# Kernel tuning notes

Measured on AMD Instinct MI355X. Metric: run time of the kernel, lower is better.

## Reference

```python
import jax, jax.numpy as jnp
import numpy as np

EPS = 1e-12


def setup_inputs() -> dict:
    key = jax.random.key(0)
    k1, k2, k3, k4 = jax.random.split(key, 4)
    N, H, W, D, K = 64, 32, 32, 512, 64
    x = jax.random.normal(k1, (N, H, W, D), dtype=jnp.float32)
    W_assign = jax.random.normal(k2, (D, K), dtype=jnp.float32) * 0.05  # 1x1 conv kernel
    b_assign = jax.random.normal(k3, (K,), dtype=jnp.float32) * 0.05
    C = jax.random.normal(k4, (D, K), dtype=jnp.float32) * 0.05  # cluster centers
    return {"x": x, "W_assign": W_assign, "b_assign": b_assign, "C": C}


def _l2norm(v, axis):
    return v / jnp.sqrt(jnp.sum(v * v, axis=axis, keepdims=True) + EPS)


def reference(x, W_assign, b_assign, C):
    # 1x1 conv = matmul over channel dim: [N,H,W,D] @ [D,K] -> [N,H,W,K]
    s = jnp.einsum('nhwd,dk->nhwk', x, W_assign) + b_assign
    a = jax.nn.softmax(s, axis=-1)                       # soft assignment over K
    # VLAD: v[n,d,k] = sum_hw a[n,h,w,k] * (x[n,h,w,d] + C[d,k])
    # reformulated as two small contractions (no [N,H,W,D,K] intermediate):
    v = jnp.einsum('nhwd,nhwk->ndk', x, a)               # feature-weighted sums
    a_sum = jnp.sum(a, axis=(1, 2))                      # [N,K]
    v = v + a_sum[:, None, :] * C[None, :, :]            # [N,D,K]
    # intra-normalization: L2 over D per cluster (after transpose to [N,K,D])
    v = _l2norm(jnp.transpose(v, (0, 2, 1)), axis=-1)    # [N,K,D]
    v = jnp.transpose(v, (0, 2, 1))                      # [N,D,K]
    # flatten and final L2 normalize -> [N, D*K]
    v = v.reshape(v.shape[0], -1)
    return _l2norm(v, axis=-1)
```

## Files before the change

kernel.cpp:

```cpp
#include <hip/hip_runtime.h>


#define EPSF 1e-12f

typedef short bf16x8 __attribute__((ext_vector_type(8)));
typedef float f32x16 __attribute__((ext_vector_type(16)));

__device__ inline unsigned short f2bf_rne(float f) {
  union { float f; unsigned u; } v; v.f = f;
  unsigned u = v.u;
  unsigned r = u + 0x7fffu + ((u >> 16) & 1u);
  return (unsigned short)(r >> 16);
}
__device__ inline unsigned pk2(float a, float b) {
  return (unsigned)f2bf_rne(a) | ((unsigned)f2bf_rne(b) << 16);
}

__global__ __launch_bounds__(256) void kprep(
    const float* __restrict__ Wm, unsigned short* __restrict__ wt) {
  __shared__ float tile[64][65];
  const int t = threadIdx.x, bx = blockIdx.x;
  {
    int col = (t & 15) * 4, rbase = t >> 4;
#pragma unroll
    for (int r = 0; r < 4; ++r) {
      int row = rbase + 16 * r;
      *(float4*)&tile[row][col] =
          *(const float4*)&Wm[(size_t)(bx * 64 + row) * 64 + col];
    }
  }
  __syncthreads();
  int k = t >> 2, seg = (t & 3) * 16;
  size_t o = (size_t)k * 512 + bx * 64 + seg;
#pragma unroll
  for (int j = 0; j < 16; j += 2)
    *(unsigned*)&wt[o + j] = pk2(tile[seg + j][k], tile[seg + j + 1][k]);
}

__global__ __launch_bounds__(256) void kassign(
    const float* __restrict__ x, const unsigned short* __restrict__ wt,
    const float* __restrict__ b, unsigned short* __restrict__ at,
    float* __restrict__ a_sum) {
  __shared__ unsigned short xs[128][72];
  __shared__ unsigned short ws[64][72];
  const int t = threadIdx.x;
  const int w = t >> 6, lane = t & 63, l31 = lane & 31, h = lane >> 5;
  const int p0 = blockIdx.x * 128;
  const int col = (t & 15) * 4, rbase = t >> 4;
  const int wk = t >> 2, wseg = (t & 3) * 16;

  float4 px[8];
  uint4 pw0, pw1;
#pragma unroll
  for (int r = 0; r < 8; ++r)
    px[r] = *(const float4*)&x[(size_t)(p0 + rbase + 16 * r) * 512 + col];
  pw0 = *(const uint4*)&wt[(size_t)wk * 512 + wseg];
  pw1 = *(const uint4*)&wt[(size_t)wk * 512 + wseg + 8];

  f32x16 acc0, acc1;
#pragma unroll
  for (int i = 0; i < 16; ++i) { acc0[i] = 0.f; acc1[i] = 0.f; }

  for (int c = 0; c < 8; ++c) {
    __syncthreads();
#pragma unroll
    for (int r = 0; r < 8; ++r) {
      uint2 ph;
      ph.x = pk2(px[r].x, px[r].y);
      ph.y = pk2(px[r].z, px[r].w);
      *(uint2*)&xs[rbase + 16 * r][col] = ph;
    }
    *(uint4*)&ws[wk][wseg] = pw0;
    *(uint4*)&ws[wk][wseg + 8] = pw1;
    __syncthreads();
    if (c < 7) {
      const int dc = (c + 1) * 64;
#pragma unroll
      for (int r = 0; r < 8; ++r)
        px[r] = *(const float4*)&x[(size_t)(p0 + rbase + 16 * r) * 512 + dc + col];
      pw0 = *(const uint4*)&wt[(size_t)wk * 512 + dc + wseg];
      pw1 = *(const uint4*)&wt[(size_t)wk * 512 + dc + wseg + 8];
    }
#pragma unroll
    for (int s = 0; s < 4; ++s) {
      int kd = s * 16 + h * 8;
      bf16x8 ax = *(const bf16x8*)&xs[32 * w + l31][kd];
      bf16x8 b0 = *(const bf16x8*)&ws[l31][kd];
      bf16x8 b1 = *(const bf16x8*)&ws[32 + l31][kd];
      acc0 = __builtin_amdgcn_mfma_f32_32x32x16_bf16(ax, b0, acc0, 0, 0, 0);
      acc1 = __builtin_amdgcn_mfma_f32_32x32x16_bf16(ax, b1, acc1, 0, 0, 0);
    }
  }

  const float bias0 = b[l31], bias1 = b[32 + l31];
  float a0[16], a1[16];
  float sum0 = 0.f, sum1 = 0.f;
#pragma unroll
  for (int r = 0; r < 16; ++r) {
    float s0 = acc0[r] + bias0, s1 = acc1[r] + bias1;
    float m = fmaxf(s0, s1);
#pragma unroll
    for (int msk = 1; msk < 32; msk <<= 1) m = fmaxf(m, __shfl_xor(m, msk, 64));
    float e0 = __expf(s0 - m), e1 = __expf(s1 - m);
    float S = e0 + e1;
#pragma unroll
    for (int msk = 1; msk < 32; msk <<= 1) S += __shfl_xor(S, msk, 64);
    float inv = 1.0f / S;
    a0[r] = e0 * inv; a1[r] = e1 * inv;
    sum0 += a0[r]; sum1 += a1[r];
  }
  const int n = p0 >> 10;
  const int hwb = (p0 & 1023) + 32 * w + 4 * h;
  const size_t kb0 = ((size_t)n * 64 + l31) * 1024;
  const size_t kb1 = ((size_t)n * 64 + 32 + l31) * 1024;
#pragma unroll
  for (int g = 0; g < 4; ++g) {
    int hw = hwb + 8 * g;
    uint2 u;
    u.x = pk2(a0[4 * g + 0], a0[4 * g + 1]);
    u.y = pk2(a0[4 * g + 2], a0[4 * g + 3]);
    *(uint2*)&at[kb0 + hw] = u;
    u.x = pk2(a1[4 * g + 0], a1[4 * g + 1]);
    u.y = pk2(a1[4 * g + 2], a1[4 * g + 3]);
    *(uint2*)&at[kb1 + hw] = u;
  }
  sum0 += __shfl_xor(sum0, 32, 64);
  sum1 += __shfl_xor(sum1, 32, 64);
  if (lane < 32) {
    atomicAdd(&a_sum[n * 64 + l31], sum0);
    atomicAdd(&a_sum[n * 64 + 32 + l31], sum1);
  }
}

__global__ __launch_bounds__(256) void kvlad(
    const float* __restrict__ x, const unsigned short* __restrict__ at,
    const float* __restrict__ a_sum, const float* __restrict__ C,
    float* __restrict__ out, float* __restrict__ ssq) {
  __shared__ float xs[64][68];
  __shared__ unsigned short as_[64][72];
  const int t = threadIdx.x;
  const int w = t >> 6, lane = t & 63, l31 = lane & 31, h = lane >> 5;
  const int n = blockIdx.y, d0 = blockIdx.x * 64;
  const int dw = 32 * (w & 1), kw = 32 * (w >> 1);
  const float* xb = x + (size_t)n * 1024 * 512;
  const int col = (t & 15) * 4, rbase = t >> 4;
  const int ak = t >> 2, aseg = (t & 3) * 16;
  const size_t abase = ((size_t)n * 64 + ak) * 1024;

  float4 px[4];
  uint4 pa0, pa1;
#pragma unroll
  for (int r = 0; r < 4; ++r)
    px[r] = *(const float4*)&xb[(size_t)(rbase + 16 * r) * 512 + d0 + col];
  pa0 = *(const uint4*)&at[abase + aseg];
  pa1 = *(const uint4*)&at[abase + aseg + 8];

  f32x16 acc;
#pragma unroll
  for (int i = 0; i < 16; ++i) acc[i] = 0.f;

  for (int c = 0; c < 16; ++c) {
    __syncthreads();
#pragma unroll
    for (int r = 0; r < 4; ++r)
      *(float4*)&xs[rbase + 16 * r][col] = px[r];
    *(uint4*)&as_[ak][aseg] = pa0;
    *(uint4*)&as_[ak][aseg + 8] = pa1;
    __syncthreads();
    if (c < 15) {
      const int hw0 = (c + 1) * 64;
#pragma unroll
      for (int r = 0; r < 4; ++r)
        px[r] = *(const float4*)&xb[(size_t)(hw0 + rbase + 16 * r) * 512 + d0 + col];
      pa0 = *(const uint4*)&at[abase + hw0 + aseg];
      pa1 = *(const uint4*)&at[abase + hw0 + aseg + 8];
    }
#pragma unroll
    for (int s = 0; s < 4; ++s) {
      int kk = s * 16 + h * 8;
      bf16x8 ax;
#pragma unroll
      for (int j = 0; j < 8; ++j)
        ax[j] = (short)f2bf_rne(xs[kk + j][dw + l31]);
      bf16x8 bh = *(const bf16x8*)&as_[kw + l31][kk];
      acc = __builtin_amdgcn_mfma_f32_32x32x16_bf16(ax, bh, acc, 0, 0, 0);
    }
  }

  const int k = kw + l31;
  const float as = a_sum[n * 64 + k];
  float sq = 0.f;
#pragma unroll
  for (int r = 0; r < 16; ++r) {
    int row = (r & 3) + 8 * (r >> 2) + 4 * h;
    int d = d0 + dw + row;
    float o = acc[r] + as * C[(size_t)d * 64 + k];
    out[((size_t)n * 512 + d) * 64 + k] = o;
    sq += o * o;
  }
  atomicAdd(&ssq[n * 64 + k], sq);
}

__global__ __launch_bounds__(256) void kscale(
    float* __restrict__ out, const float* __restrict__ ssq) {
  const int n = blockIdx.y, slice = blockIdx.x;
  const int t = threadIdx.x, k = t & 63, rg = t >> 6;
  __shared__ float sk[64];
  __shared__ float tot;
  if (t < 64) {
    float c = ssq[n * 64 + t];
    sk[t] = rsqrtf(c + EPSF);
    float contrib = c / (c + EPSF);
#pragma unroll
    for (int m = 32; m; m >>= 1) contrib += __shfl_xor(contrib, m, 64);
    if (t == 0) tot = rsqrtf(contrib + EPSF);
  }
  __syncthreads();
  const float scale = sk[k] * tot;
  float* vb = out + (size_t)n * 32768 + (size_t)slice * 4096;
#pragma unroll
  for (int r = rg; r < 64; r += 4) vb[r * 64 + k] *= scale;
}

extern "C" void kernel_launch(void* const* d_in, const int* in_sizes, int n_in,
                              void* d_out, int out_size, void* d_ws, size_t ws_size,
                              hipStream_t stream) {
  const float* x  = (const float*)d_in[0];
  const float* Wm = (const float*)d_in[1];
  const float* b  = (const float*)d_in[2];
  const float* C  = (const float*)d_in[3];
  float* out = (float*)d_out;

  unsigned short* at = (unsigned short*)d_ws;
  unsigned short* wt = at + (size_t)64 * 64 * 1024;
  float* a_sum = (float*)(wt + (size_t)64 * 512);
  float* ssq   = a_sum + 4096;

  hipMemsetAsync(a_sum, 0, 8192 * sizeof(float), stream);
  kprep<<<dim3(8), dim3(256), 0, stream>>>(Wm, wt);
  kassign<<<dim3(512), dim3(256), 0, stream>>>(x, wt, b, at, a_sum);
  kvlad<<<dim3(8, 64), dim3(256), 0, stream>>>(x, at, a_sum, C, out, ssq);
  kscale<<<dim3(8, 64), dim3(256), 0, stream>>>(out, ssq);
}
```

Baseline: 274.4 us.

## Pre-transpose x to bf16 [N,D,HW] layout for the VLAD contraction

Adds a kernel that converts x to bf16 and transposes it to a D-major, HW-contiguous layout in workspace. The VLAD kernel then loads bf16 rows with vector LDS reads, replacing strided fp32 LDS reads and per-element bf16 conversion in the inner loop. This costs an extra full pass over x (128 MB read, 64 MB written) while kvlad reads half as many bytes of x.

```diff
diff --git a/kernel.cpp b/kernel.cpp
--- a/kernel.cpp
+++ b/kernel.cpp
@@ -35,6 +35,33 @@
 #pragma unroll
   for (int j = 0; j < 16; j += 2)
     *(unsigned*)&wt[o + j] = pk2(tile[seg + j][k], tile[seg + j + 1][k]);
+}
+
+__global__ __launch_bounds__(256) void kconv(
+    const float* __restrict__ x, unsigned short* __restrict__ xt) {
+  __shared__ unsigned short td[64][66];
+  const int t = threadIdx.x;
+  const int hw0 = (blockIdx.x & 15) * 64, d0 = (blockIdx.x >> 4) * 64;
+  const int n = blockIdx.y;
+  {
+    int c = (t & 15) * 4, r0 = t >> 4;
+#pragma unroll
+    for (int rr = 0; rr < 4; ++rr) {
+      int row = r0 + 16 * rr;
+      float4 v = *(const float4*)&x[((size_t)(n * 1024 + hw0 + row)) * 512 + d0 + c];
+      *(unsigned*)&td[row][c] = pk2(v.x, v.y);
+      *(unsigned*)&td[row][c + 2] = pk2(v.z, v.w);
+    }
+  }
+  __syncthreads();
+  const int d = t >> 2, hs = (t & 3) * 16;
+  unsigned o[8];
+#pragma unroll
+  for (int j = 0; j < 8; ++j)
+    o[j] = (unsigned)td[hs + 2 * j][d] | ((unsigned)td[hs + 2 * j + 1][d] << 16);
+  size_t g = ((size_t)n * 512 + d0 + d) * 1024 + hw0 + hs;
+  *(uint4*)&xt[g] = *(uint4*)&o[0];
+  *(uint4*)&xt[g + 8] = *(uint4*)&o[4];
 }
 
 __global__ __launch_bounds__(256) void kassign(
@@ -133,27 +160,24 @@
 }
 
 __global__ __launch_bounds__(256) void kvlad(
-    const float* __restrict__ x, const unsigned short* __restrict__ at,
+    const unsigned short* __restrict__ xt, const unsigned short* __restrict__ at,
     const float* __restrict__ a_sum, const float* __restrict__ C,
     float* __restrict__ out, float* __restrict__ ssq) {
-  __shared__ float xs[64][68];
+  __shared__ unsigned short xa[64][72];
   __shared__ unsigned short as_[64][72];
   const int t = threadIdx.x;
   const int w = t >> 6, lane = t & 63, l31 = lane & 31, h = lane >> 5;
   const int n = blockIdx.y, d0 = blockIdx.x * 64;
   const int dw = 32 * (w & 1), kw = 32 * (w >> 1);
-  const float* xb = x + (size_t)n * 1024 * 512;
-  const int col = (t & 15) * 4, rbase = t >> 4;
-  const int ak = t >> 2, aseg = (t & 3) * 16;
-  const size_t abase = ((size_t)n * 64 + ak) * 1024;
-
-  float4 px[4];
-  uint4 pa0, pa1;
-#pragma unroll
-  for (int r = 0; r < 4; ++r)
-    px[r] = *(const float4*)&xb[(size_t)(rbase + 16 * r) * 512 + d0 + col];
-  pa0 = *(const uint4*)&at[abase + aseg];
-  pa1 = *(const uint4*)&at[abase + aseg + 8];
+  const int sd = t >> 2, sseg = (t & 3) * 16;
+  const size_t xbase = ((size_t)n * 512 + d0 + sd) * 1024;
+  const size_t abase = ((size_t)n * 64 + sd) * 1024;
+
+  uint4 px0, px1, pa0, pa1;
+  px0 = *(const uint4*)&xt[xbase + sseg];
+  px1 = *(const uint4*)&xt[xbase + sseg + 8];
+  pa0 = *(const uint4*)&at[abase + sseg];
+  pa1 = *(const uint4*)&at[abase + sseg + 8];
 
   f32x16 acc;
 #pragma unroll
@@ -161,29 +185,24 @@
 
   for (int c = 0; c < 16; ++c) {
     __syncthreads();
-#pragma unroll
-    for (int r = 0; r < 4; ++r)
-      *(float4*)&xs[rbase + 16 * r][col] = px[r];
-    *(uint4*)&as_[ak][aseg] = pa0;
-    *(uint4*)&as_[ak][aseg + 8] = pa1;
+    *(uint4*)&xa[sd][sseg] = px0;
+    *(uint4*)&xa[sd][sseg + 8] = px1;
+    *(uint4*)&as_[sd][sseg] = pa0;
+    *(uint4*)&as_[sd][sseg + 8] = pa1;
     __syncthreads();
     if (c < 15) {
       const int hw0 = (c + 1) * 64;
-#pragma unroll
-      for (int r = 0; r < 4; ++r)
-        px[r] = *(const float4*)&xb[(size_t)(hw0 + rbase + 16 * r) * 512 + d0 + col];
-      pa0 = *(const uint4*)&at[abase + hw0 + aseg];
-      pa1 = *(const uint4*)&at[abase + hw0 + aseg + 8];
+      px0 = *(const uint4*)&xt[xbase + hw0 + sseg];
+      px1 = *(const uint4*)&xt[xbase + hw0 + sseg + 8];
+      pa0 = *(const uint4*)&at[abase + hw0 + sseg];
+      pa1 = *(const uint4*)&at[abase + hw0 + sseg + 8];
     }
 #pragma unroll
     for (int s = 0; s < 4; ++s) {
       int kk = s * 16 + h * 8;
-      bf16x8 ax;
-#pragma unroll
-      for (int j = 0; j < 8; ++j)
-        ax[j] = (short)f2bf_rne(xs[kk + j][dw + l31]);
-      bf16x8 bh = *(const bf16x8*)&as_[kw + l31][kk];
-      acc = __builtin_amdgcn_mfma_f32_32x32x16_bf16(ax, bh, acc, 0, 0, 0);
+      bf16x8 ax = *(const bf16x8*)&xa[dw + l31][kk];
+      bf16x8 bb = *(const bf16x8*)&as_[kw + l31][kk];
+      acc = __builtin_amdgcn_mfma_f32_32x32x16_bf16(ax, bb, acc, 0, 0, 0);
     }
   }
 
@@ -232,13 +251,15 @@
   float* out = (float*)d_out;
 
   unsigned short* at = (unsigned short*)d_ws;
-  unsigned short* wt = at + (size_t)64 * 64 * 1024;
+  unsigned short* xt = at + (size_t)64 * 64 * 1024;
+  unsigned short* wt = xt + (size_t)64 * 512 * 1024;
   float* a_sum = (float*)(wt + (size_t)64 * 512);
   float* ssq   = a_sum + 4096;
 
   hipMemsetAsync(a_sum, 0, 8192 * sizeof(float), stream);
   kprep<<<dim3(8), dim3(256), 0, stream>>>(Wm, wt);
+  kconv<<<dim3(128, 64), dim3(256), 0, stream>>>(x, xt);
   kassign<<<dim3(512), dim3(256), 0, stream>>>(x, wt, b, at, a_sum);
-  kvlad<<<dim3(8, 64), dim3(256), 0, stream>>>(x, at, a_sum, C, out, ssq);
+  kvlad<<<dim3(8, 64), dim3(256), 0, stream>>>(xt, at, a_sum, C, out, ssq);
   kscale<<<dim3(8, 64), dim3(256), 0, stream>>>(out, ssq);
 }
```

Measured after the change: 260.4 us. -5.1%, faster.

## Drop LDS staging in GEMM kernels, load MFMA operands straight from global

Applied to the files above, without the earlier changes.

Both the assignment and VLAD kernels now read their MFMA operands straight from global memory into registers instead of staging tiles through shared memory with barriers. The stats buffer is zeroed by an extra block of the prep kernel rather than a separate memset, and pk2 uses a hardware bf16 pack conversion when one is available. The aim is to remove LDS traffic, syncthreads and one launch. The risk is that the VLAD kernel now does strided scalar global loads (stride 512 floats per element) and the assign kernel loses cross-wave reuse of the weight tile, both leaning on cache coalescing.

```diff
diff --git a/kernel.cpp b/kernel.cpp
--- a/kernel.cpp
+++ b/kernel.cpp
@@ -13,13 +13,34 @@
   return (unsigned short)(r >> 16);
 }
 __device__ inline unsigned pk2(float a, float b) {
+#if __has_builtin(__builtin_amdgcn_cvt_pk_bf16_f32)
+  auto r = __builtin_amdgcn_cvt_pk_bf16_f32(a, b);
+  return __builtin_bit_cast(unsigned, r);
+#else
   return (unsigned)f2bf_rne(a) | ((unsigned)f2bf_rne(b) << 16);
+#endif
+}
+__device__ inline bf16x8 pack8(float4 lo, float4 hi) {
+  union { unsigned u[4]; bf16x8 v; } r;
+  r.u[0] = pk2(lo.x, lo.y);
+  r.u[1] = pk2(lo.z, lo.w);
+  r.u[2] = pk2(hi.x, hi.y);
+  r.u[3] = pk2(hi.z, hi.w);
+  return r.v;
 }
 
 __global__ __launch_bounds__(256) void kprep(
-    const float* __restrict__ Wm, unsigned short* __restrict__ wt) {
+    const float* __restrict__ Wm, unsigned short* __restrict__ wt,
+    float* __restrict__ stats ) {
+  const int t = threadIdx.x, bx = blockIdx.x;
+  if (bx == 8) {
+    float4 z = {0.f, 0.f, 0.f, 0.f};
+#pragma unroll
+    for (int r = 0; r < 8; ++r)
+      *(float4*)&stats[(size_t)(r * 256 + t) * 4] = z;
+    return;
+  }
   __shared__ float tile[64][65];
-  const int t = threadIdx.x, bx = blockIdx.x;
   {
     int col = (t & 15) * 4, rbase = t >> 4;
 #pragma unroll
@@ -41,55 +62,29 @@
     const float* __restrict__ x, const unsigned short* __restrict__ wt,
     const float* __restrict__ b, unsigned short* __restrict__ at,
     float* __restrict__ a_sum) {
-  __shared__ unsigned short xs[128][72];
-  __shared__ unsigned short ws[64][72];
   const int t = threadIdx.x;
   const int w = t >> 6, lane = t & 63, l31 = lane & 31, h = lane >> 5;
-  const int p0 = blockIdx.x * 128;
-  const int col = (t & 15) * 4, rbase = t >> 4;
-  const int wk = t >> 2, wseg = (t & 3) * 16;
-
-  float4 px[8];
-  uint4 pw0, pw1;
-#pragma unroll
-  for (int r = 0; r < 8; ++r)
-    px[r] = *(const float4*)&x[(size_t)(p0 + rbase + 16 * r) * 512 + col];
-  pw0 = *(const uint4*)&wt[(size_t)wk * 512 + wseg];
-  pw1 = *(const uint4*)&wt[(size_t)wk * 512 + wseg + 8];
+  const int bx = blockIdx.x;
+  const int n = bx >> 3;
+  const int hwbase = (bx & 7) * 128 + 32 * w;
+  const size_t prow = (size_t)(bx * 128 + 32 * w + l31) * 512;
+  const unsigned short* w0 = wt + (size_t)l31 * 512;
+  const unsigned short* w1 = wt + (size_t)(32 + l31) * 512;
 
   f32x16 acc0, acc1;
 #pragma unroll
   for (int i = 0; i < 16; ++i) { acc0[i] = 0.f; acc1[i] = 0.f; }
 
-  for (int c = 0; c < 8; ++c) {
-    __syncthreads();
-#pragma unroll
-    for (int r = 0; r < 8; ++r) {
-      uint2 ph;
-      ph.x = pk2(px[r].x, px[r].y);
-      ph.y = pk2(px[r].z, px[r].w);
-      *(uint2*)&xs[rbase + 16 * r][col] = ph;
-    }
-    *(uint4*)&ws[wk][wseg] = pw0;
-    *(uint4*)&ws[wk][wseg + 8] = pw1;
-    __syncthreads();
-    if (c < 7) {
-      const int dc = (c + 1) * 64;
-#pragma unroll
-      for (int r = 0; r < 8; ++r)
-        px[r] = *(const float4*)&x[(size_t)(p0 + rbase + 16 * r) * 512 + dc + col];
-      pw0 = *(const uint4*)&wt[(size_t)wk * 512 + dc + wseg];
-      pw1 = *(const uint4*)&wt[(size_t)wk * 512 + dc + wseg + 8];
-    }
-#pragma unroll
-    for (int s = 0; s < 4; ++s) {
-      int kd = s * 16 + h * 8;
-      bf16x8 ax = *(const bf16x8*)&xs[32 * w + l31][kd];
-      bf16x8 b0 = *(const bf16x8*)&ws[l31][kd];
-      bf16x8 b1 = *(const bf16x8*)&ws[32 + l31][kd];
-      acc0 = __builtin_amdgcn_mfma_f32_32x32x16_bf16(ax, b0, acc0, 0, 0, 0);
-      acc1 = __builtin_amdgcn_mfma_f32_32x32x16_bf16(ax, b1, acc1, 0, 0, 0);
-    }
+#pragma unroll 8
+  for (int st = 0; st < 32; ++st) {
+    const int kd = st * 16 + h * 8;
+    float4 xa = *(const float4*)&x[prow + kd];
+    float4 xb = *(const float4*)&x[prow + kd + 4];
+    bf16x8 ax = pack8(xa, xb);
+    bf16x8 b0 = *(const bf16x8*)&w0[kd];
+    bf16x8 b1 = *(const bf16x8*)&w1[kd];
+    acc0 = __builtin_amdgcn_mfma_f32_32x32x16_bf16(ax, b0, acc0, 0, 0, 0);
+    acc1 = __builtin_amdgcn_mfma_f32_32x32x16_bf16(ax, b1, acc1, 0, 0, 0);
   }
 
   const float bias0 = b[l31], bias1 = b[32 + l31];
@@ -109,8 +104,7 @@
     a0[r] = e0 * inv; a1[r] = e1 * inv;
     sum0 += a0[r]; sum1 += a1[r];
   }
-  const int n = p0 >> 10;
-  const int hwb = (p0 & 1023) + 32 * w + 4 * h;
+  const int hwb = hwbase + 4 * h;
   const size_t kb0 = ((size_t)n * 64 + l31) * 1024;
   const size_t kb1 = ((size_t)n * 64 + 32 + l31) * 1024;
 #pragma unroll
@@ -136,55 +130,31 @@
     const float* __restrict__ x, const unsigned short* __restrict__ at,
     const float* __restrict__ a_sum, const float* __restrict__ C,
     float* __restrict__ out, float* __restrict__ ssq) {
-  __shared__ float xs[64][68];
-  __shared__ unsigned short as_[64][72];
   const int t = threadIdx.x;
   const int w = t >> 6, lane = t & 63, l31 = lane & 31, h = lane >> 5;
   const int n = blockIdx.y, d0 = blockIdx.x * 64;
   const int dw = 32 * (w & 1), kw = 32 * (w >> 1);
-  const float* xb = x + (size_t)n * 1024 * 512;
-  const int col = (t & 15) * 4, rbase = t >> 4;
-  const int ak = t >> 2, aseg = (t & 3) * 16;
-  const size_t abase = ((size_t)n * 64 + ak) * 1024;
-
-  float4 px[4];
-  uint4 pa0, pa1;
-#pragma unroll
-  for (int r = 0; r < 4; ++r)
-    px[r] = *(const float4*)&xb[(size_t)(rbase + 16 * r) * 512 + d0 + col];
-  pa0 = *(const uint4*)&at[abase + aseg];
-  pa1 = *(const uint4*)&at[abase + aseg + 8];
+  const int d = d0 + dw + l31;
+  const float* xl = x + (size_t)n * 524288 + d;
+  const unsigned short* al = at + ((size_t)n * 64 + kw + l31) * 1024;
 
   f32x16 acc;
 #pragma unroll
   for (int i = 0; i < 16; ++i) acc[i] = 0.f;
 
-  for (int c = 0; c < 16; ++c) {
-    __syncthreads();
-#pragma unroll
-    for (int r = 0; r < 4; ++r)
-      *(float4*)&xs[rbase + 16 * r][col] = px[r];
-    *(uint4*)&as_[ak][aseg] = pa0;
-    *(uint4*)&as_[ak][aseg + 8] = pa1;
-    __syncthreads();
-    if (c < 15) {
-      const int hw0 = (c + 1) * 64;
-#pragma unroll
-      for (int r = 0; r < 4; ++r)
-        px[r] = *(const float4*)&xb[(size_t)(hw0 + rbase + 16 * r) * 512 + d0 + col];
-      pa0 = *(const uint4*)&at[abase + hw0 + aseg];
-      pa1 = *(const uint4*)&at[abase + hw0 + aseg + 8];
-    }
-#pragma unroll
-    for (int s = 0; s < 4; ++s) {
-      int kk = s * 16 + h * 8;
-      bf16x8 ax;
-#pragma unroll
-      for (int j = 0; j < 8; ++j)
-        ax[j] = (short)f2bf_rne(xs[kk + j][dw + l31]);
-      bf16x8 bh = *(const bf16x8*)&as_[kw + l31][kk];
-      acc = __builtin_amdgcn_mfma_f32_32x32x16_bf16(ax, bh, acc, 0, 0, 0);
-    }
+#pragma unroll 4
+  for (int m = 0; m < 64; ++m) {
+    const int hwb = m * 16 + h * 8;
+    float a[8];
+#pragma unroll
+    for (int j = 0; j < 8; ++j) a[j] = xl[(size_t)(hwb + j) * 512];
+    union { unsigned u[4]; bf16x8 v; } ax;
+    ax.u[0] = pk2(a[0], a[1]);
+    ax.u[1] = pk2(a[2], a[3]);
+    ax.u[2] = pk2(a[4], a[5]);
+    ax.u[3] = pk2(a[6], a[7]);
+    bf16x8 bb = *(const bf16x8*)&al[hwb];
+    acc = __builtin_amdgcn_mfma_f32_32x32x16_bf16(ax.v, bb, acc, 0, 0, 0);
   }
 
   const int k = kw + l31;
@@ -193,9 +163,9 @@
 #pragma unroll
   for (int r = 0; r < 16; ++r) {
     int row = (r & 3) + 8 * (r >> 2) + 4 * h;
-    int d = d0 + dw + row;
-    float o = acc[r] + as * C[(size_t)d * 64 + k];
-    out[((size_t)n * 512 + d) * 64 + k] = o;
+    int dd = d0 + dw + row;
+    float o = acc[r] + as * C[(size_t)dd * 64 + k];
+    out[((size_t)n * 512 + dd) * 64 + k] = o;
     sq += o * o;
   }
   atomicAdd(&ssq[n * 64 + k], sq);
@@ -233,11 +203,11 @@
 
   unsigned short* at = (unsigned short*)d_ws;
   unsigned short* wt = at + (size_t)64 * 64 * 1024;
-  float* a_sum = (float*)(wt + (size_t)64 * 512);
-  float* ssq   = a_sum + 4096;
-
-  hipMemsetAsync(a_sum, 0, 8192 * sizeof(float), stream);
-  kprep<<<dim3(8), dim3(256), 0, stream>>>(Wm, wt);
+  float* stats = (float*)(wt + (size_t)64 * 512);
+  float* a_sum = stats;
+  float* ssq   = stats + 4096;
+
+  kprep<<<dim3(9), dim3(256), 0, stream>>>(Wm, wt, stats);
   kassign<<<dim3(512), dim3(256), 0, stream>>>(x, wt, b, at, a_sum);
   kvlad<<<dim3(8, 64), dim3(256), 0, stream>>>(x, at, a_sum, C, out, ssq);
   kscale<<<dim3(8, 64), dim3(256), 0, stream>>>(out, ssq);
```

Measured after the change: 245.5 us. 10.5% less time.
